# Kernel tuning notes

Hardware: AMD Instinct MI355X
Metric: run time of the kernel (lower is better)

The kernel has to match this reference:

```python
import jax, jax.numpy as jnp
import numpy as np

MAXDISP = 25               # module stores maxdisp + 1
OFFSET = (MAXDISP - 1) // 2  # center of the residual disparity range


def setup_inputs() -> dict:
    key = jax.random.key(0)
    k1, k2 = jax.random.split(key)
    x = jax.random.normal(k1, (8, 32, 256, 512), dtype=jnp.float32)
    y = jax.random.normal(k2, (8, 32, 256, 512), dtype=jnp.float32)
    return {"x": x, "y": y}


def reference(x, y):
    # Residual cost volume: for each centered disparity shift d, the cost slice
    # is the channel-wise L1 distance between x and y shifted by d along width,
    # with zeros in the out-of-overlap columns.
    N, C, H, W = x.shape
    slices = []
    for i in range(MAXDISP):  # small fixed loop over disparity hypotheses
        d = i - OFFSET
        if d < 0:
            # overlap occupies columns [0, W+d); right -d columns are zero
            c = jnp.abs(x[..., : W + d] - y[..., -d:]).sum(axis=1)
            c = jnp.pad(c, ((0, 0), (0, 0), (0, -d)))
        elif d > 0:
            # overlap occupies columns [d, W); left d columns are zero
            c = jnp.abs(x[..., d:] - y[..., : W - d]).sum(axis=1)
            c = jnp.pad(c, ((0, 0), (0, 0), (d, 0)))
        else:
            c = jnp.abs(x - y).sum(axis=1)
        slices.append(c)  # (N, H, W)
    return jnp.stack(slices, axis=1)  # (N, MAXDISP, H, W)
```

## Files before the change

kernel.cpp:

```cpp
#include <hip/hip_runtime.h>

namespace {
constexpr int N_ = 8, C_ = 32, H_ = 256, W_ = 512, DISP_ = 25;
constexpr int CH = H_ * W_;
constexpr int NSS = C_ / 2;
}

typedef const __attribute__((address_space(1))) void gas_t;
typedef __attribute__((address_space(3))) void las_t;

template <int DG>
__device__ __forceinline__ void body(const float* __restrict__ sbase,
                                     float* __restrict__ op, float* lds,
                                     int lds_woff, const int* yoff, int w0) {
  constexpr int NI = 13 - DG;
  constexpr int I0 = 13 * DG;

  float acc[NI][4];
#pragma unroll
  for (int il = 0; il < NI; ++il)
#pragma unroll
    for (int cw = 0; cw < 4; ++cw) acc[il][cw] = 0.0f;

#define STAGE(s)                                                          \
  do {                                                                    \
    __builtin_amdgcn_global_load_lds(                                     \
        (gas_t*)(sbase + (size_t)(2 * (s)) * CH),                         \
        (las_t*)(lds + ((s)&3) * 2048 + lds_woff), 16, 0, 0);             \
    __builtin_amdgcn_global_load_lds(                                     \
        (gas_t*)(sbase + (size_t)(2 * (s) + 1) * CH),                     \
        (las_t*)(lds + ((s)&3) * 2048 + 1024 + lds_woff), 16, 0, 0);      \
  } while (0)

#define COMPUTE1(base)                                                    \
  do {                                                                    \
    const float* lx = (base);                     \
    const float* ly = (base) + 512;               \
    const float4 xv = *reinterpret_cast<const float4*>(lx + w0);          \
    float4 yv[4];                                                         \
    _Pragma("unroll") for (int k = 0; k < 4; ++k) yv[k] =                 \
        *reinterpret_cast<const float4*>(ly + yoff[k]);                   \
    const float xs[4] = {xv.x, xv.y, xv.z, xv.w};                         \
    const float ywin[16] = {yv[0].x, yv[0].y, yv[0].z, yv[0].w,           \
                            yv[1].x, yv[1].y, yv[1].z, yv[1].w,           \
                            yv[2].x, yv[2].y, yv[2].z, yv[2].w,           \
                            yv[3].x, yv[3].y, yv[3].z, yv[3].w};          \
    _Pragma("unroll") for (int il = 0; il < NI; ++il) {                   \
      _Pragma("unroll") for (int cw = 0; cw < 4; ++cw) {                  \
        acc[il][cw] += fabsf(xs[cw] - ywin[cw + 12 - DG - il]);           \
      }                                                                   \
    }                                                                     \
  } while (0)

#define COMPUTE2(s)                                                       \
  do {                                                                    \
    const float* bp = lds + ((s)&3) * 2048;                               \
    COMPUTE1(bp);                                                         \
    COMPUTE1(bp + 1024);                                                  \
  } while (0)

  STAGE(0);
  STAGE(1);

#pragma unroll 1
  for (int s = 0; s < NSS - 1; ++s) {
    asm volatile("s_waitcnt vmcnt(2)" ::: "memory");
    __builtin_amdgcn_s_barrier();
    if (s + 2 < NSS) STAGE(s + 2);
    COMPUTE2(s);
  }
  asm volatile("s_waitcnt vmcnt(0)" ::: "memory");
  __builtin_amdgcn_s_barrier();
  COMPUTE2(NSS - 1);

#undef STAGE
#undef COMPUTE1
#undef COMPUTE2

#pragma unroll
  for (int il = 0; il < NI; ++il) {
    const int i = I0 + il;
    const int j0 = w0 - i + 12;
    float4 v;
    v.x = ((unsigned)(j0 + 0) < (unsigned)W_) ? acc[il][0] : 0.0f;
    v.y = ((unsigned)(j0 + 1) < (unsigned)W_) ? acc[il][1] : 0.0f;
    v.z = ((unsigned)(j0 + 2) < (unsigned)W_) ? acc[il][2] : 0.0f;
    v.w = ((unsigned)(j0 + 3) < (unsigned)W_) ? acc[il][3] : 0.0f;
    *reinterpret_cast<float4*>(op + (size_t)i * CH) = v;
  }
}

__global__ __launch_bounds__(256, 4) void rescost_kernel(
    const float* __restrict__ x, const float* __restrict__ y,
    float* __restrict__ out) {
  __shared__ __align__(16) float lds[4 * 2048];

  const int tid = threadIdx.x;
  const int t = tid & 127;
  const int dg = tid >> 7;
  const int wv = tid >> 6;
  const int lane = tid & 63;
  const int r = blockIdx.x;
  const int n = r >> 8;
  const int h = r & (H_ - 1);
  const int w0 = t << 2;

  const size_t row_base = ((size_t)n * C_ * H_ + (size_t)h) * W_;
  const float* sbase =
      ((wv < 2) ? x : y) + row_base + ((wv & 1) << 8) + (lane << 2);
  const int lds_woff = ((wv >> 1) << 9) + ((wv & 1) << 8);

  int yoff[4];
  const int ybase = w0 - 12 * dg;
#pragma unroll
  for (int k = 0; k < 4; ++k) {
    int idx = ybase + 4 * k;
    idx = idx < 0 ? 0 : idx;
    idx = idx > (W_ - 4) ? (W_ - 4) : idx;
    yoff[k] = idx;
  }

  float* op = out + ((size_t)n * DISP_ * H_ + (size_t)h) * W_ + w0;

  if (dg == 0)
    body<0>(sbase, op, lds, lds_woff, yoff, w0);
  else
    body<1>(sbase, op, lds, lds_woff, yoff, w0);
}

extern "C" void kernel_launch(void* const* d_in, const int* in_sizes, int n_in,
                              void* d_out, int out_size, void* d_ws, size_t ws_size,
                              hipStream_t stream) {
  const float* x = (const float*)d_in[0];
  const float* y = (const float*)d_in[1];
  float* out = (float*)d_out;
  dim3 grid(N_ * H_);
  dim3 block(256);
  hipLaunchKernelGGL(rescost_kernel, grid, block, 0, stream, x, y, out);
}
```

Baseline: 81.34 us.

## Split disparity work across four thread groups with 512-thread blocks

Doubles the block to 512 threads and splits the 25 disparities across four groups of 128 threads (7/6/6/6) instead of two groups (13/12). Each thread now loads a 12-wide y window (3 float4) instead of 16, which cuts register pressure. Each wave issues a single global-to-LDS load per stage, so the wait count drops to vmcnt(1). The aim is more parallelism and more waves to hide latency, at the cost of more redundant LDS x reads per block and larger barrier groups.

```diff
diff --git a/kernel.cpp b/kernel.cpp
--- a/kernel.cpp
+++ b/kernel.cpp
@@ -9,12 +9,13 @@
 typedef const __attribute__((address_space(1))) void gas_t;
 typedef __attribute__((address_space(3))) void las_t;
 
-template <int DG>
+template <int G>
 __device__ __forceinline__ void body(const float* __restrict__ sbase,
                                      float* __restrict__ op, float* lds,
                                      int lds_woff, const int* yoff, int w0) {
-  constexpr int NI = 13 - DG;
-  constexpr int I0 = 13 * DG;
+  constexpr int I0 = (G == 0) ? 0 : (G == 1) ? 7 : (G == 2) ? 13 : 19;
+  constexpr int NI = (G == 0) ? 7 : 6;
+  constexpr int OFF = (G == 0) ? 4 : (G == 1) ? 0 : (G == 2) ? -8 : -12;
 
   float acc[NI][4];
 #pragma unroll
@@ -23,31 +24,25 @@
     for (int cw = 0; cw < 4; ++cw) acc[il][cw] = 0.0f;
 
 #define STAGE(s)                                                          \
-  do {                                                                    \
-    __builtin_amdgcn_global_load_lds(                                     \
-        (gas_t*)(sbase + (size_t)(2 * (s)) * CH),                         \
-        (las_t*)(lds + ((s)&3) * 2048 + lds_woff), 16, 0, 0);             \
-    __builtin_amdgcn_global_load_lds(                                     \
-        (gas_t*)(sbase + (size_t)(2 * (s) + 1) * CH),                     \
-        (las_t*)(lds + ((s)&3) * 2048 + 1024 + lds_woff), 16, 0, 0);      \
-  } while (0)
+  __builtin_amdgcn_global_load_lds(                                       \
+      (gas_t*)(sbase + (size_t)(2 * (s)) * CH),                           \
+      (las_t*)(lds + ((s)&3) * 2048 + lds_woff), 16, 0, 0)
 
 #define COMPUTE1(base)                                                    \
   do {                                                                    \
     const float* lx = (base);                     \
     const float* ly = (base) + 512;               \
     const float4 xv = *reinterpret_cast<const float4*>(lx + w0);          \
-    float4 yv[4];                                                         \
-    _Pragma("unroll") for (int k = 0; k < 4; ++k) yv[k] =                 \
+    float4 yv[3];                                                         \
+    _Pragma("unroll") for (int k = 0; k < 3; ++k) yv[k] =                 \
         *reinterpret_cast<const float4*>(ly + yoff[k]);                   \
     const float xs[4] = {xv.x, xv.y, xv.z, xv.w};                         \
-    const float ywin[16] = {yv[0].x, yv[0].y, yv[0].z, yv[0].w,           \
+    const float ywin[12] = {yv[0].x, yv[0].y, yv[0].z, yv[0].w,           \
                             yv[1].x, yv[1].y, yv[1].z, yv[1].w,           \
-                            yv[2].x, yv[2].y, yv[2].z, yv[2].w,           \
-                            yv[3].x, yv[3].y, yv[3].z, yv[3].w};          \
+                            yv[2].x, yv[2].y, yv[2].z, yv[2].w};          \
     _Pragma("unroll") for (int il = 0; il < NI; ++il) {                   \
       _Pragma("unroll") for (int cw = 0; cw < 4; ++cw) {                  \
-        acc[il][cw] += fabsf(xs[cw] - ywin[cw + 12 - DG - il]);           \
+        acc[il][cw] += fabsf(xs[cw] - ywin[cw + 12 - OFF - (I0 + il)]);   \
       }                                                                   \
     }                                                                     \
   } while (0)
@@ -64,7 +59,7 @@
 
 #pragma unroll 1
   for (int s = 0; s < NSS - 1; ++s) {
-    asm volatile("s_waitcnt vmcnt(2)" ::: "memory");
+    asm volatile("s_waitcnt vmcnt(1)" ::: "memory");
     __builtin_amdgcn_s_barrier();
     if (s + 2 < NSS) STAGE(s + 2);
     COMPUTE2(s);
@@ -90,14 +85,14 @@
   }
 }
 
-__global__ __launch_bounds__(256, 4) void rescost_kernel(
+__global__ __launch_bounds__(512, 4) void rescost_kernel(
     const float* __restrict__ x, const float* __restrict__ y,
     float* __restrict__ out) {
   __shared__ __align__(16) float lds[4 * 2048];
 
   const int tid = threadIdx.x;
   const int t = tid & 127;
-  const int dg = tid >> 7;
+  const int g = tid >> 7;
   const int wv = tid >> 6;
   const int lane = tid & 63;
   const int r = blockIdx.x;
@@ -105,15 +100,19 @@
   const int h = r & (H_ - 1);
   const int w0 = t << 2;
 
+  const int arr = wv & 1;
+  const int chsel = (wv >> 1) & 1;
+  const int half = wv >> 2;
   const size_t row_base = ((size_t)n * C_ * H_ + (size_t)h) * W_;
-  const float* sbase =
-      ((wv < 2) ? x : y) + row_base + ((wv & 1) << 8) + (lane << 2);
-  const int lds_woff = ((wv >> 1) << 9) + ((wv & 1) << 8);
+  const float* sbase = (arr ? y : x) + row_base + (size_t)chsel * CH +
+                       (half << 8) + (lane << 2);
+  const int lds_woff = (chsel << 10) + (arr << 9) + (half << 8);
 
-  int yoff[4];
-  const int ybase = w0 - 12 * dg;
+  const int off_tab[4] = {4, 0, -8, -12};
+  const int ybase = w0 + off_tab[g];
+  int yoff[3];
 #pragma unroll
-  for (int k = 0; k < 4; ++k) {
+  for (int k = 0; k < 3; ++k) {
     int idx = ybase + 4 * k;
     idx = idx < 0 ? 0 : idx;
     idx = idx > (W_ - 4) ? (W_ - 4) : idx;
@@ -122,10 +121,14 @@
 
   float* op = out + ((size_t)n * DISP_ * H_ + (size_t)h) * W_ + w0;
 
-  if (dg == 0)
+  if (g == 0)
     body<0>(sbase, op, lds, lds_woff, yoff, w0);
+  else if (g == 1)
+    body<1>(sbase, op, lds, lds_woff, yoff, w0);
+  else if (g == 2)
+    body<2>(sbase, op, lds, lds_woff, yoff, w0);
   else
-    body<1>(sbase, op, lds, lds_woff, yoff, w0);
+    body<3>(sbase, op, lds, lds_woff, yoff, w0);
 }
 
 extern "C" void kernel_launch(void* const* d_in, const int* in_sizes, int n_in,
@@ -135,6 +138,6 @@
   const float* y = (const float*)d_in[1];
   float* out = (float*)d_out;
   dim3 grid(N_ * H_);
-  dim3 block(256);
+  dim3 block(512);
   hipLaunchKernelGGL(rescost_kernel, grid, block, 0, stream, x, y, out);
 }
```

New measurement: 83.79 us. 1.03x slower.
